# Performance work log

Measured on AMD Instinct MI355X. Metric: run time of the kernel, lower is better.

## Reference

```python
import jax, jax.numpy as jnp
import numpy as np

HIDDEN = 2048
INTER = 5632
TOKENS = 8192


def _hadamard(n: int) -> np.ndarray:
    # Sylvester construction, normalized so H @ H.T = I
    H = np.array([[1.0]], dtype=np.float32)
    while H.shape[0] < n:
        H = np.block([[H, H], [H, -H]])
    return (H / np.sqrt(n)).astype(np.float32)


def setup_inputs() -> dict:
    key = jax.random.key(0)
    kx, kg, ku, kd = jax.random.split(key, 4)
    x = jax.random.normal(kx, (TOKENS, HIDDEN), dtype=jnp.float32)
    H = jnp.asarray(_hadamard(HIDDEN))
    s_in = 1.0 / np.sqrt(HIDDEN)
    s_mid = 1.0 / np.sqrt(INTER)
    # gate/up weights are the pre-rotated weights (rotation folded in at init);
    # random init stands in for the rotated values.
    gate_w = jax.random.normal(kg, (INTER, HIDDEN), dtype=jnp.float32) * s_in
    up_w = jax.random.normal(ku, (INTER, HIDDEN), dtype=jnp.float32) * s_in
    down_w = jax.random.normal(kd, (HIDDEN, INTER), dtype=jnp.float32) * s_mid
    return {"x": x, "H": H, "gate_w": gate_w, "up_w": up_w, "down_w": down_w}


def reference(x, H, gate_w, up_w, down_w):
    # Hadamard rotation in fp32, cast back to input dtype
    x_rot = (x.astype(jnp.float32) @ H.T).astype(x.dtype)  # [T, hidden]
    # Qwen2 expert MLP (SwiGLU): down( silu(gate(x)) * up(x) )
    g = jax.nn.silu(x_rot @ gate_w.T)  # [T, inter]
    u = x_rot @ up_w.T                 # [T, inter]
    return (g * u) @ down_w.T          # [T, hidden]
```

## Files before the change

kernel.cpp:

```cpp
#include <hip/hip_runtime.h>
#include <math.h>

#define HIDDEN 2048
#define INTER  5632
#define TOKENS 8192

typedef __attribute__((ext_vector_type(8))) short bf16x8;
typedef __attribute__((ext_vector_type(4))) float f32x4;
typedef __attribute__((ext_vector_type(4))) short short4v;

#define FENCE() asm volatile("" ::: "memory")
#define BAR()   __builtin_amdgcn_s_barrier()
#define LGKM0() asm volatile("s_waitcnt lgkmcnt(0)" ::: "memory")
#define SCHED0() __builtin_amdgcn_sched_barrier(0)
#define VMCNT(n) asm volatile("s_waitcnt vmcnt(" #n ")" ::: "memory")

__device__ __forceinline__ short f2bf(float f) {
  union { float f; unsigned u; } v; v.f = f;
  unsigned r = v.u + 0x7fffu + ((v.u >> 16) & 1u);
  return (short)(r >> 16);
}
__device__ __forceinline__ float bf2f(short s) {
  union { unsigned u; float f; } v; v.u = ((unsigned)(unsigned short)s) << 16;
  return v.f;
}

__global__ __launch_bounds__(256) void cvt_w(const float* __restrict__ src,
                                             short* __restrict__ dst, int n4) {
  int i = blockIdx.x * 256 + threadIdx.x;
  if (i >= n4) return;
  float4 v = ((const float4*)src)[i];
  short4v o;
  o[0] = f2bf(v.x); o[1] = f2bf(v.y); o[2] = f2bf(v.z); o[3] = f2bf(v.w);
  ((short4v*)dst)[i] = o;
}

__global__ __launch_bounds__(256) void fwht_cast(const float* __restrict__ X,
                                                 short* __restrict__ Xr) {
  __shared__ __align__(16) float row[HIDDEN];
  const int tid = threadIdx.x;
  for (int r = blockIdx.x; r < TOKENS; r += gridDim.x) {
    const float4* src = (const float4*)(X + (size_t)r * HIDDEN);
    float4 va = src[tid];
    float4 vb = src[tid + 256];
    float a[8] = {va.x, va.y, va.z, va.w, vb.x, vb.y, vb.z, vb.w};
    #pragma unroll
    for (int j = 0; j < 4; ++j) { float s = a[j] + a[j+4], d = a[j] - a[j+4]; a[j] = s; a[j+4] = d; }
    #pragma unroll
    for (int j = 0; j < 8; j += 2) { float s = a[j] + a[j+1], d = a[j] - a[j+1]; a[j] = s; a[j+1] = d; }
    #pragma unroll
    for (int h = 0; h < 8; h += 4) {
      { float s = a[h]   + a[h+2], d = a[h]   - a[h+2]; a[h]   = s; a[h+2] = d; }
      { float s = a[h+1] + a[h+3], d = a[h+1] - a[h+3]; a[h+1] = s; a[h+3] = d; }
    }
    ((float4*)row)[tid]       = make_float4(a[0], a[1], a[2], a[3]);
    ((float4*)row)[tid + 256] = make_float4(a[4], a[5], a[6], a[7]);
    __syncthreads();
    for (int s = 4; s <= 512; s <<= 1) {
      #pragma unroll
      for (int pp = 0; pp < 4; ++pp) {
        int p = tid + pp * 256;
        int i = ((p & ~(s - 1)) << 1) | (p & (s - 1));
        float x0 = row[i], x1 = row[i + s];
        row[i] = x0 + x1; row[i + s] = x0 - x1;
      }
      __syncthreads();
    }
    const float scale = 0.02209708691207961f;
    float4 wa = ((float4*)row)[tid];
    float4 wb = ((float4*)row)[tid + 256];
    short4v oa, ob;
    oa[0] = f2bf(wa.x * scale); oa[1] = f2bf(wa.y * scale);
    oa[2] = f2bf(wa.z * scale); oa[3] = f2bf(wa.w * scale);
    ob[0] = f2bf(wb.x * scale); ob[1] = f2bf(wb.y * scale);
    ob[2] = f2bf(wb.z * scale); ob[3] = f2bf(wb.w * scale);
    short* dst = Xr + (size_t)r * HIDDEN;
    ((short4v*)dst)[tid]       = oa;
    ((short4v*)dst)[tid + 256] = ob;
    __syncthreads();
  }
}

__device__ __forceinline__ void stage_half(const short* __restrict__ gbase, int ldK, int kt,
                                           short* region, int tid) {
  const int w = tid >> 6;
  #pragma unroll
  for (int j = 0; j < 2; ++j) {
    const int slot = tid + j * 512;
    const int row  = slot >> 3;
    const int cg   = (slot & 7) ^ (row & 7);
    const short* gp = gbase + (size_t)row * ldK + kt * 64 + cg * 8;
    short* lp = region + w * 512 + j * 4096;
    __builtin_amdgcn_global_load_lds((const __attribute__((address_space(1))) void*)gp,
                                     (__attribute__((address_space(3))) void*)lp, 16, 0, 0);
  }
}

__device__ __forceinline__ void ldsA(const short* rg, int qm, int fr, const int* cx,
                                     bf16x8* dst) {
  #pragma unroll
  for (int i = 0; i < 4; ++i)
    #pragma unroll
    for (int kk = 0; kk < 2; ++kk)
      dst[i * 2 + kk] = *(const bf16x8*)(rg + (qm * 64 + i * 16 + fr) * 64 + cx[kk]);
}

__device__ __forceinline__ void ldsB(const short* rg, int qn, int rb, int fr, const int* cx,
                                     bf16x8* dst) {
  #pragma unroll
  for (int n = 0; n < 2; ++n)
    #pragma unroll
    for (int kk = 0; kk < 2; ++kk)
      dst[n * 2 + kk] = *(const bf16x8*)(rg + (rb + qn * 32 + n * 16 + fr) * 64 + cx[kk]);
}

__device__ __forceinline__ void mfma16(const bf16x8* a, const bf16x8* b,
                                       f32x4 (&acc)[8][4], int qm, int qn) {
  #pragma unroll
  for (int i = 0; i < 4; ++i)
    #pragma unroll
    for (int n = 0; n < 2; ++n)
      #pragma unroll
      for (int kk = 0; kk < 2; ++kk)
        acc[qm * 4 + i][qn * 2 + n] = __builtin_amdgcn_mfma_f32_16x16x32_bf16(
            a[i * 2 + kk], b[n * 2 + kk], acc[qm * 4 + i][qn * 2 + n], 0, 0, 0);
}

template<int LDK, int NBN, int NOUT, int EPI>
__global__ __launch_bounds__(512, 2) void gemm256(const short* __restrict__ A,
                                                  const short* __restrict__ B,
                                                  void* __restrict__ Cv) {
  constexpr int NKT = LDK / 64;
  constexpr int NITER = NKT / 2;
  __shared__ __align__(16) short lds[2][4][8192];

  const int tid  = threadIdx.x;
  const int lane = tid & 63, wv = tid >> 6;
  const int wr = wv >> 2, wc = wv & 3;
  const int fr = lane & 15, fq = lane >> 4;
  const int x7 = fr & 7;
  const int cx[2] = { (fq ^ x7) * 8, ((4 + fq) ^ x7) * 8 };
  const int rbB = (wc & 1) * 64;

  const int nwg = gridDim.x;
  const int swz = (blockIdx.x & 7) * (nwg >> 3) + (blockIdx.x >> 3);
  const int bm = swz / NBN, bn = swz % NBN;

  const short* Ab[2] = { A + (size_t)(bm * 256) * LDK, A + (size_t)(bm * 256 + 128) * LDK };
  const short* Bb[2] = { B + (size_t)(bn * 256) * LDK, B + (size_t)(bn * 256 + 128) * LDK };

#define STAGE(kt_, rg_) stage_half((rg_) < 2 ? Ab[(rg_)] : Bb[(rg_) - 2], LDK, (kt_), \
                                   &lds[(kt_) & 1][(rg_)][0], tid)

  f32x4 acc[8][4] = {};

  STAGE(0, 0); STAGE(0, 1); STAGE(0, 2); STAGE(0, 3);
  STAGE(1, 0); STAGE(1, 1); STAGE(1, 2);
  VMCNT(6);
  FENCE(); BAR();

  bf16x8 af0[8], af1[8], bf0[4], bf1[4];

  for (int it = 0; it < NITER; ++it) {
    const int e = 2 * it;
    const bool nl = (it < NITER - 1);
    const short* Ar0 = &lds[0][wr][0];
    const short* Br0 = &lds[0][2 + (wc >> 1)][0];
    const short* Ar1 = &lds[1][wr][0];
    const short* Br1 = &lds[1][2 + (wc >> 1)][0];

    ldsA(Ar0, 0, fr, cx, af0);
    ldsB(Br0, 0, rbB, fr, cx, bf0);
    STAGE(e + 1, 3);
    FENCE(); BAR(); LGKM0(); SCHED0();
    __builtin_amdgcn_s_setprio(1); mfma16(af0, bf0, acc, 0, 0); __builtin_amdgcn_s_setprio(0);
    FENCE(); BAR();

    ldsA(Ar0, 1, fr, cx, af1);
    if (nl) STAGE(e + 2, 0);
    FENCE(); BAR(); LGKM0(); SCHED0();
    __builtin_amdgcn_s_setprio(1); mfma16(af1, bf0, acc, 1, 0); __builtin_amdgcn_s_setprio(0);
    FENCE(); BAR();

    ldsB(Br0, 1, rbB, fr, cx, bf1);
    if (nl) STAGE(e + 2, 1);
    FENCE(); BAR(); LGKM0(); SCHED0();
    __builtin_amdgcn_s_setprio(1); mfma16(af1, bf1, acc, 1, 1); __builtin_amdgcn_s_setprio(0);
    FENCE(); BAR();

    if (nl) STAGE(e + 2, 2);
    FENCE(); BAR(); LGKM0(); SCHED0();
    __builtin_amdgcn_s_setprio(1); mfma16(af0, bf1, acc, 0, 1); __builtin_amdgcn_s_setprio(0);
    if (nl) { VMCNT(6); } else { VMCNT(0); }
    FENCE(); BAR();

    ldsA(Ar1, 0, fr, cx, af0);
    ldsB(Br1, 0, rbB, fr, cx, bf0);
    if (nl) STAGE(e + 2, 3);
    FENCE(); BAR(); LGKM0(); SCHED0();
    __builtin_amdgcn_s_setprio(1); mfma16(af0, bf0, acc, 0, 0); __builtin_amdgcn_s_setprio(0);
    FENCE(); BAR();

    ldsA(Ar1, 1, fr, cx, af1);
    if (nl) STAGE(e + 3, 0);
    FENCE(); BAR(); LGKM0(); SCHED0();
    __builtin_amdgcn_s_setprio(1); mfma16(af1, bf0, acc, 1, 0); __builtin_amdgcn_s_setprio(0);
    FENCE(); BAR();

    ldsB(Br1, 1, rbB, fr, cx, bf1);
    if (nl) STAGE(e + 3, 1);
    FENCE(); BAR(); LGKM0(); SCHED0();
    __builtin_amdgcn_s_setprio(1); mfma16(af1, bf1, acc, 1, 1); __builtin_amdgcn_s_setprio(0);
    FENCE(); BAR();

    if (nl) STAGE(e + 3, 2);
    FENCE(); BAR(); LGKM0(); SCHED0();
    __builtin_amdgcn_s_setprio(1); mfma16(af0, bf1, acc, 0, 1); __builtin_amdgcn_s_setprio(0);
    if (nl) { VMCNT(6); }
    FENCE(); BAR();
  }
#undef STAGE

  const int rowb = bm * 256 + wr * 128 + fq * 4;
  const int colb = bn * 256 + wc * 64 + fr;
  #pragma unroll
  for (int m = 0; m < 8; ++m) {
    #pragma unroll
    for (int nf = 0; nf < 4; ++nf) {
      #pragma unroll
      for (int ii = 0; ii < 4; ++ii) {
        const size_t idx = (size_t)(rowb + m * 16 + ii) * NOUT + (colb + nf * 16);
        float v = acc[m][nf][ii];
        if (EPI == 0) {
          ((short*)Cv)[idx] = f2bf(v / (1.0f + __expf(-v)));
        } else if (EPI == 1) {
          float sg = bf2f(((const short*)Cv)[idx]);
          ((short*)Cv)[idx] = f2bf(v * sg);
        } else {
          ((float*)Cv)[idx] = v;
        }
      }
    }
  }
}

extern "C" void kernel_launch(void* const* d_in, const int* in_sizes, int n_in,
                              void* d_out, int out_size, void* d_ws, size_t ws_size,
                              hipStream_t stream) {
  const float* x      = (const float*)d_in[0];
  const float* gate_w = (const float*)d_in[2];
  const float* up_w   = (const float*)d_in[3];
  const float* down_w = (const float*)d_in[4];
  float* out = (float*)d_out;

  short* xr = (short*)d_ws;
  short* gw = xr + (size_t)TOKENS * HIDDEN;
  short* uw = gw + (size_t)INTER * HIDDEN;
  short* dw = uw + (size_t)INTER * HIDDEN;
  short* sg = dw + (size_t)HIDDEN * INTER;

  const int n4 = (INTER * HIDDEN) / 4;
  cvt_w<<<(n4 + 255) / 256, 256, 0, stream>>>(gate_w, gw, n4);
  cvt_w<<<(n4 + 255) / 256, 256, 0, stream>>>(up_w, uw, n4);
  cvt_w<<<(n4 + 255) / 256, 256, 0, stream>>>(down_w, dw, n4);

  fwht_cast<<<2048, 256, 0, stream>>>(x, xr);

  gemm256<HIDDEN, INTER / 256, INTER, 0>
      <<<(TOKENS / 256) * (INTER / 256), 512, 0, stream>>>(xr, gw, sg);
  gemm256<HIDDEN, INTER / 256, INTER, 1>
      <<<(TOKENS / 256) * (INTER / 256), 512, 0, stream>>>(xr, uw, sg);
  gemm256<INTER, HIDDEN / 256, HIDDEN, 2>
      <<<(TOKENS / 256) * (HIDDEN / 256), 512, 0, stream>>>(sg, dw, out);
}
```

Measured before the change: 719.9 us.

## Fuse gate and up GEMMs with SwiGLU epilogue and merge weight conversion launches

Replaces the separate gate and up GEMMs, whose second epilogue re-read the gate activations, with one kernel. Each block loads an A tile plus 128-column tiles of both gate and up weights and applies silu(g)*u before writing bf16. The three weight-cast kernels become a single launch, and the fwht grid doubles. The k-loop is restructured to one k-tile per iteration, and the explicit lgkmcnt waits and sched barriers are removed in favour of fence/barrier pairs. This risks compiler-inserted waits changing the overlap of LDS reads and MFMA.

```diff
diff --git a/kernel.cpp b/kernel.cpp
--- a/kernel.cpp
+++ b/kernel.cpp
@@ -11,9 +11,10 @@
 
 #define FENCE() asm volatile("" ::: "memory")
 #define BAR()   __builtin_amdgcn_s_barrier()
-#define LGKM0() asm volatile("s_waitcnt lgkmcnt(0)" ::: "memory")
-#define SCHED0() __builtin_amdgcn_sched_barrier(0)
 #define VMCNT(n) asm volatile("s_waitcnt vmcnt(" #n ")" ::: "memory")
+#define PRIO1() __builtin_amdgcn_s_setprio(1)
+#define PRIO0() __builtin_amdgcn_s_setprio(0)
+#define BARF()  do { FENCE(); BAR(); FENCE(); } while (0)
 
 __device__ __forceinline__ short f2bf(float f) {
   union { float f; unsigned u; } v; v.f = f;
@@ -25,11 +26,16 @@
   return v.f;
 }
 
-__global__ __launch_bounds__(256) void cvt_w(const float* __restrict__ src,
-                                             short* __restrict__ dst, int n4) {
+__global__ __launch_bounds__(256) void cvt_all(const float* __restrict__ g,
+                                               const float* __restrict__ u,
+                                               const float* __restrict__ d,
+                                               short* __restrict__ dst, int n4) {
   int i = blockIdx.x * 256 + threadIdx.x;
-  if (i >= n4) return;
-  float4 v = ((const float4*)src)[i];
+  const float* src; int off;
+  if (i < n4)            { src = g; off = i; }
+  else if (i < 2 * n4)   { src = u; off = i - n4; }
+  else                   { src = d; off = i - 2 * n4; }
+  float4 v = ((const float4*)src)[off];
   short4v o;
   o[0] = f2bf(v.x); o[1] = f2bf(v.y); o[2] = f2bf(v.z); o[3] = f2bf(v.w);
   ((short4v*)dst)[i] = o;
@@ -114,8 +120,29 @@
       dst[n * 2 + kk] = *(const bf16x8*)(rg + (rb + qn * 32 + n * 16 + fr) * 64 + cx[kk]);
 }
 
-__device__ __forceinline__ void mfma16(const bf16x8* a, const bf16x8* b,
-                                       f32x4 (&acc)[8][4], int qm, int qn) {
+__device__ __forceinline__ void ldsB32(const short* rg, int wc, int fr, const int* cx,
+                                       bf16x8* dst) {
+  #pragma unroll
+  for (int n = 0; n < 2; ++n)
+    #pragma unroll
+    for (int kk = 0; kk < 2; ++kk)
+      dst[n * 2 + kk] = *(const bf16x8*)(rg + (wc * 32 + n * 16 + fr) * 64 + cx[kk]);
+}
+
+__device__ __forceinline__ void mfma_ph2(const bf16x8* a, const bf16x8* b,
+                                         f32x4 (&acc)[8][2], int qm) {
+  #pragma unroll
+  for (int i = 0; i < 4; ++i)
+    #pragma unroll
+    for (int n = 0; n < 2; ++n)
+      #pragma unroll
+      for (int kk = 0; kk < 2; ++kk)
+        acc[qm * 4 + i][n] = __builtin_amdgcn_mfma_f32_16x16x32_bf16(
+            a[i * 2 + kk], b[n * 2 + kk], acc[qm * 4 + i][n], 0, 0, 0);
+}
+
+__device__ __forceinline__ void mfma_ph4(const bf16x8* a, const bf16x8* b,
+                                         f32x4 (&acc)[8][4], int qm, int qn) {
   #pragma unroll
   for (int i = 0; i < 4; ++i)
     #pragma unroll
@@ -126,12 +153,98 @@
             a[i * 2 + kk], b[n * 2 + kk], acc[qm * 4 + i][qn * 2 + n], 0, 0, 0);
 }
 
-template<int LDK, int NBN, int NOUT, int EPI>
-__global__ __launch_bounds__(512, 2) void gemm256(const short* __restrict__ A,
-                                                  const short* __restrict__ B,
-                                                  void* __restrict__ Cv) {
+template<int LDK, int NBN>
+__global__ __launch_bounds__(512, 2) void gemm_gateup(const short* __restrict__ A,
+                                                      const short* __restrict__ Bg,
+                                                      const short* __restrict__ Bu,
+                                                      short* __restrict__ Hb) {
   constexpr int NKT = LDK / 64;
-  constexpr int NITER = NKT / 2;
+  __shared__ __align__(16) short lds[2][4][8192];
+
+  const int tid  = threadIdx.x;
+  const int lane = tid & 63, wv = tid >> 6;
+  const int wr = wv >> 2, wc = wv & 3;
+  const int fr = lane & 15, fq = lane >> 4;
+  const int x7 = fr & 7;
+  const int cx[2] = { (fq ^ x7) * 8, ((4 + fq) ^ x7) * 8 };
+
+  const int nwg = gridDim.x;
+  const int swz = (blockIdx.x & 7) * (nwg >> 3) + (blockIdx.x >> 3);
+  const int bm = swz / NBN, bn = swz % NBN;
+
+  const short* Ab[2] = { A + (size_t)(bm * 256) * LDK, A + (size_t)(bm * 256 + 128) * LDK };
+  const short* Bgb = Bg + (size_t)(bn * 128) * LDK;
+  const short* Bub = Bu + (size_t)(bn * 128) * LDK;
+
+#define STAGE(kt_, rg_) stage_half((rg_) == 0 ? Ab[0] : (rg_) == 1 ? Ab[1] : \
+                                   (rg_) == 2 ? Bgb : Bub, LDK, (kt_), \
+                                   &lds[(kt_) & 1][(rg_)][0], tid)
+
+  f32x4 accG[8][2] = {};
+  f32x4 accU[8][2] = {};
+
+  STAGE(0, 0); STAGE(0, 1); STAGE(0, 2); STAGE(0, 3);
+  STAGE(1, 0); STAGE(1, 1); STAGE(1, 2);
+  VMCNT(6);
+  BARF();
+
+  bf16x8 af0[8], af1[8], bg[4], bu[4];
+
+  for (int kt = 0; kt < NKT; ++kt) {
+    const bool nl1 = (kt + 1 < NKT), nl2 = (kt + 2 < NKT);
+    const short* Ar  = &lds[kt & 1][wr][0];
+    const short* Bgr = &lds[kt & 1][2][0];
+    const short* Bur = &lds[kt & 1][3][0];
+
+    ldsA(Ar, 0, fr, cx, af0);
+    ldsB32(Bgr, wc, fr, cx, bg);
+    ldsA(Ar, 1, fr, cx, af1);
+    if (nl1) STAGE(kt + 1, 3);
+    BARF();
+    PRIO1(); mfma_ph2(af0, bg, accG, 0); PRIO0();
+    BARF();
+
+    ldsB32(Bur, wc, fr, cx, bu);
+    if (nl2) STAGE(kt + 2, 0);
+    BARF();
+    PRIO1(); mfma_ph2(af1, bg, accG, 1); PRIO0();
+    BARF();
+
+    if (nl2) STAGE(kt + 2, 1);
+    BARF();
+    PRIO1(); mfma_ph2(af1, bu, accU, 1); PRIO0();
+    BARF();
+
+    if (nl2) STAGE(kt + 2, 2);
+    BARF();
+    PRIO1(); mfma_ph2(af0, bu, accU, 0); PRIO0();
+    if (nl2) { VMCNT(6); } else if (nl1) { VMCNT(0); }
+    BARF();
+  }
+#undef STAGE
+
+  const int rowb = bm * 256 + wr * 128 + fq * 4;
+  const int colb = bn * 128 + wc * 32 + fr;
+  #pragma unroll
+  for (int m = 0; m < 8; ++m) {
+    #pragma unroll
+    for (int nf = 0; nf < 2; ++nf) {
+      #pragma unroll
+      for (int ii = 0; ii < 4; ++ii) {
+        const size_t idx = (size_t)(rowb + m * 16 + ii) * INTER + (colb + nf * 16);
+        float g = accG[m][nf][ii];
+        float u = accU[m][nf][ii];
+        Hb[idx] = f2bf(g * u / (1.0f + __expf(-g)));
+      }
+    }
+  }
+}
+
+template<int LDK, int NBN>
+__global__ __launch_bounds__(512, 2) void gemm_down(const short* __restrict__ A,
+                                                    const short* __restrict__ B,
+                                                    float* __restrict__ Out) {
+  constexpr int NKT = LDK / 64;
   __shared__ __align__(16) short lds[2][4][8192];
 
   const int tid  = threadIdx.x;
@@ -157,67 +270,39 @@
   STAGE(0, 0); STAGE(0, 1); STAGE(0, 2); STAGE(0, 3);
   STAGE(1, 0); STAGE(1, 1); STAGE(1, 2);
   VMCNT(6);
-  FENCE(); BAR();
+  BARF();
 
   bf16x8 af0[8], af1[8], bf0[4], bf1[4];
 
-  for (int it = 0; it < NITER; ++it) {
-    const int e = 2 * it;
-    const bool nl = (it < NITER - 1);
-    const short* Ar0 = &lds[0][wr][0];
-    const short* Br0 = &lds[0][2 + (wc >> 1)][0];
-    const short* Ar1 = &lds[1][wr][0];
-    const short* Br1 = &lds[1][2 + (wc >> 1)][0];
-
-    ldsA(Ar0, 0, fr, cx, af0);
-    ldsB(Br0, 0, rbB, fr, cx, bf0);
-    STAGE(e + 1, 3);
-    FENCE(); BAR(); LGKM0(); SCHED0();
-    __builtin_amdgcn_s_setprio(1); mfma16(af0, bf0, acc, 0, 0); __builtin_amdgcn_s_setprio(0);
-    FENCE(); BAR();
-
-    ldsA(Ar0, 1, fr, cx, af1);
-    if (nl) STAGE(e + 2, 0);
-    FENCE(); BAR(); LGKM0(); SCHED0();
-    __builtin_amdgcn_s_setprio(1); mfma16(af1, bf0, acc, 1, 0); __builtin_amdgcn_s_setprio(0);
-    FENCE(); BAR();
-
-    ldsB(Br0, 1, rbB, fr, cx, bf1);
-    if (nl) STAGE(e + 2, 1);
-    FENCE(); BAR(); LGKM0(); SCHED0();
-    __builtin_amdgcn_s_setprio(1); mfma16(af1, bf1, acc, 1, 1); __builtin_amdgcn_s_setprio(0);
-    FENCE(); BAR();
-
-    if (nl) STAGE(e + 2, 2);
-    FENCE(); BAR(); LGKM0(); SCHED0();
-    __builtin_amdgcn_s_setprio(1); mfma16(af0, bf1, acc, 0, 1); __builtin_amdgcn_s_setprio(0);
-    if (nl) { VMCNT(6); } else { VMCNT(0); }
-    FENCE(); BAR();
-
-    ldsA(Ar1, 0, fr, cx, af0);
-    ldsB(Br1, 0, rbB, fr, cx, bf0);
-    if (nl) STAGE(e + 2, 3);
-    FENCE(); BAR(); LGKM0(); SCHED0();
-    __builtin_amdgcn_s_setprio(1); mfma16(af0, bf0, acc, 0, 0); __builtin_amdgcn_s_setprio(0);
-    FENCE(); BAR();
-
-    ldsA(Ar1, 1, fr, cx, af1);
-    if (nl) STAGE(e + 3, 0);
-    FENCE(); BAR(); LGKM0(); SCHED0();
-    __builtin_amdgcn_s_setprio(1); mfma16(af1, bf0, acc, 1, 0); __builtin_amdgcn_s_setprio(0);
-    FENCE(); BAR();
-
-    ldsB(Br1, 1, rbB, fr, cx, bf1);
-    if (nl) STAGE(e + 3, 1);
-    FENCE(); BAR(); LGKM0(); SCHED0();
-    __builtin_amdgcn_s_setprio(1); mfma16(af1, bf1, acc, 1, 1); __builtin_amdgcn_s_setprio(0);
-    FENCE(); BAR();
-
-    if (nl) STAGE(e + 3, 2);
-    FENCE(); BAR(); LGKM0(); SCHED0();
-    __builtin_amdgcn_s_setprio(1); mfma16(af0, bf1, acc, 0, 1); __builtin_amdgcn_s_setprio(0);
-    if (nl) { VMCNT(6); }
-    FENCE(); BAR();
+  for (int kt = 0; kt < NKT; ++kt) {
+    const bool nl1 = (kt + 1 < NKT), nl2 = (kt + 2 < NKT);
+    const short* Ar = &lds[kt & 1][wr][0];
+    const short* Br = &lds[kt & 1][2 + (wc >> 1)][0];
+
+    ldsA(Ar, 0, fr, cx, af0);
+    ldsB(Br, 0, rbB, fr, cx, bf0);
+    ldsA(Ar, 1, fr, cx, af1);
+    if (nl1) STAGE(kt + 1, 3);
+    BARF();
+    PRIO1(); mfma_ph4(af0, bf0, acc, 0, 0); PRIO0();
+    BARF();
+
+    ldsB(Br, 1, rbB, fr, cx, bf1);
+    if (nl2) STAGE(kt + 2, 0);
+    BARF();
+    PRIO1(); mfma_ph4(af1, bf0, acc, 1, 0); PRIO0();
+    BARF();
+
+    if (nl2) STAGE(kt + 2, 1);
+    BARF();
+    PRIO1(); mfma_ph4(af1, bf1, acc, 1, 1); PRIO0();
+    BARF();
+
+    if (nl2) STAGE(kt + 2, 2);
+    BARF();
+    PRIO1(); mfma_ph4(af0, bf1, acc, 0, 1); PRIO0();
+    if (nl2) { VMCNT(6); } else if (nl1) { VMCNT(0); }
+    BARF();
   }
 #undef STAGE
 
@@ -229,16 +314,7 @@
     for (int nf = 0; nf < 4; ++nf) {
       #pragma unroll
       for (int ii = 0; ii < 4; ++ii) {
-        const size_t idx = (size_t)(rowb + m * 16 + ii) * NOUT + (colb + nf * 16);
-        float v = acc[m][nf][ii];
-        if (EPI == 0) {
-          ((short*)Cv)[idx] = f2bf(v / (1.0f + __expf(-v)));
-        } else if (EPI == 1) {
-          float sg = bf2f(((const short*)Cv)[idx]);
-          ((short*)Cv)[idx] = f2bf(v * sg);
-        } else {
-          ((float*)Cv)[idx] = v;
-        }
+        Out[(size_t)(rowb + m * 16 + ii) * HIDDEN + (colb + nf * 16)] = acc[m][nf][ii];
       }
     }
   }
@@ -257,19 +333,15 @@
   short* gw = xr + (size_t)TOKENS * HIDDEN;
   short* uw = gw + (size_t)INTER * HIDDEN;
   short* dw = uw + (size_t)INTER * HIDDEN;
-  short* sg = dw + (size_t)HIDDEN * INTER;
+  short* hb = dw + (size_t)HIDDEN * INTER;
 
   const int n4 = (INTER * HIDDEN) / 4;
-  cvt_w<<<(n4 + 255) / 256, 256, 0, stream>>>(gate_w, gw, n4);
-  cvt_w<<<(n4 + 255) / 256, 256, 0, stream>>>(up_w, uw, n4);
-  cvt_w<<<(n4 + 255) / 256, 256, 0, stream>>>(down_w, dw, n4);
-
-  fwht_cast<<<2048, 256, 0, stream>>>(x, xr);
-
-  gemm256<HIDDEN, INTER / 256, INTER, 0>
-      <<<(TOKENS / 256) * (INTER / 256), 512, 0, stream>>>(xr, gw, sg);
-  gemm256<HIDDEN, INTER / 256, INTER, 1>
-      <<<(TOKENS / 256) * (INTER / 256), 512, 0, stream>>>(xr, uw, sg);
-  gemm256<INTER, HIDDEN / 256, HIDDEN, 2>
-      <<<(TOKENS / 256) * (HIDDEN / 256), 512, 0, stream>>>(sg, dw, out);
-}
+  cvt_all<<<(3 * n4) / 256, 256, 0, stream>>>(gate_w, up_w, down_w, gw, n4);
+
+  fwht_cast<<<4096, 256, 0, stream>>>(x, xr);
+
+  gemm_gateup<HIDDEN, INTER / 128>
+      <<<(TOKENS / 256) * (INTER / 128), 512, 0, stream>>>(xr, gw, uw, hb);
+  gemm_down<INTER, HIDDEN / 256>
+      <<<(TOKENS / 256) * (HIDDEN / 256), 512, 0, stream>>>(hb, dw, out);
+}
```

After: 695.3 us. 1.04x faster.
